# Kernel tuning notes

Measured on AMD Instinct MI355X. Metric: run time of the kernel, lower is better.

## Reference

```python
import jax, jax.numpy as jnp
import numpy as np

B, SEQ_LEN, IN_DIM = 16, 1024, 768
R = 0.1
PI = 3.1415926


def conv1d(x, w, b):
    # x: [B,C,L], w: [O,I,3], 'same' padding, stride 1
    y = jax.lax.conv_general_dilated(x, w, window_strides=(1,), padding=[(1, 1)],
                                     dimension_numbers=('NCH', 'OIH', 'NCH'))
    return y + b[None, :, None]


def layernorm_cl(x, g, b, eps=1e-5):
    # torch nn.LayerNorm((C, L)): normalize jointly over the last two dims of [B,C,L]
    m = x.mean(axis=(1, 2), keepdims=True)
    v = x.var(axis=(1, 2), keepdims=True)
    return (x - m) / jnp.sqrt(v + eps) * g[None] + b[None]


def setup_inputs() -> dict:
    key = jax.random.key(0)
    ks = jax.random.split(key, 8)
    D, D2, L = IN_DIM, IN_DIM * 2, SEQ_LEN
    sc1 = 1.0 / np.sqrt(D * 3)
    sc2 = 1.0 / np.sqrt(D2 * 3)
    return {
        'feats': jax.random.normal(ks[0], (B, L, D), dtype=jnp.float32),
        'conv1_w': jax.random.normal(ks[1], (D2, D, 3), dtype=jnp.float32) * sc1,
        'conv1_b': jnp.zeros((D2,), jnp.float32),
        'ln1_w': jnp.ones((D2, L), jnp.float32),
        'ln1_b': jnp.zeros((D2, L), jnp.float32),
        'conv2_w': jax.random.normal(ks[2], (D2, D2, 3), dtype=jnp.float32) * sc2,
        'conv2_b': jnp.zeros((D2,), jnp.float32),
        'ln2_w': jnp.ones((D2, L), jnp.float32),
        'ln2_b': jnp.zeros((D2, L), jnp.float32),
        'conv3_w': jax.random.normal(ks[3], (2, D2, 3), dtype=jnp.float32) * sc2,
        'conv3_b': jnp.zeros((2,), jnp.float32),
        'ln3_w': jnp.ones((2, L), jnp.float32),
        'ln3_b': jnp.zeros((2, L), jnp.float32),
    }


def reference(feats, conv1_w, conv1_b, ln1_w, ln1_b, conv2_w, conv2_b, ln2_w, ln2_b,
              conv3_w, conv3_b, ln3_w, ln3_b):
    # NOTE: original uses nn.LeakyReLU(True) -> negative_slope=1.0, i.e. identity.
    x = jnp.transpose(feats, (0, 2, 1))                 # [B,D,L]
    h = layernorm_cl(conv1d(x, conv1_w, conv1_b), ln1_w, ln1_b)
    h = layernorm_cl(conv1d(h, conv2_w, conv2_b), ln2_w, ln2_b)
    h = layernorm_cl(conv1d(h, conv3_w, conv3_b), ln3_w, ln3_b)  # [B,2,L]
    s = jax.nn.softmax(h[:, 0, :], axis=1)              # [B,L]
    w = jax.nn.softmax(h[:, 1, :], axis=1)              # [B,L]
    # Vectorized over all centers i: std[b,i] = R*L*s[b,i]
    std = R * SEQ_LEN * s                               # [B,L]
    pos = jnp.arange(SEQ_LEN, dtype=feats.dtype)
    diff2 = (pos[None, :] - pos[:, None]) ** 2          # [i_center, j]
    c = (2.0 * PI) ** -0.5
    gauss = c / std[:, :, None] * jnp.exp(-diff2[None] / (1e-05 + 2.0 * std[:, :, None] ** 2))
    gauss = gauss / jnp.max(gauss, axis=2, keepdims=True)
    att = gauss * w[:, None, :]                         # [B,L_center,L]
    out = jnp.einsum('bij,bjd->bid', att, feats)        # [B,L,D]
    return out
```

## Files before the change

### kernel.cpp

```cpp
#include <hip/hip_runtime.h>
#include <hip/hip_bf16.h>
#include <cstdint>

#define B_   16
#define L_   1024
#define D_   768
#define D2_  1536

typedef __attribute__((ext_vector_type(8))) short bf16x8;
typedef __attribute__((ext_vector_type(4))) float f32x4;

__device__ __forceinline__ float ldin(const void* p, size_t i, int bf) {
  if (bf) return __bfloat162float(((const __hip_bfloat16*)p)[i]);
  return ((const float*)p)[i];
}
__device__ __forceinline__ unsigned short f2bs(float f) {
  __hip_bfloat16 h = __float2bfloat16(f);
  return *(unsigned short*)&h;
}
__device__ __forceinline__ float bs2f(unsigned short u) {
  __hip_bfloat16 h; *(unsigned short*)&h = u;
  return __bfloat162float(h);
}

__device__ __forceinline__ void gload16(const unsigned short* g, unsigned short* l) {
  __builtin_amdgcn_global_load_lds(
      (const __attribute__((address_space(1))) unsigned int*)g,
      (__attribute__((address_space(3))) unsigned int*)l, 16, 0, 0);
}

__global__ void k_detect(const void* __restrict__ ln1w, int* __restrict__ flag) {
  if (threadIdx.x == 0) {
    unsigned u = *(const unsigned*)ln1w;
    *flag = (u == 0x3F800000u) ? 0 : 1;
  }
}

__global__ __launch_bounds__(256) void k_cvt_x(const void* __restrict__ in,
                                               unsigned short* __restrict__ out,
                                               const int* __restrict__ flag) {
  const int bf = *flag;
  const size_t total = (size_t)B_ * (L_ + 2) * D_;
  for (size_t i = (size_t)blockIdx.x * 256 + threadIdx.x; i < total; i += (size_t)gridDim.x * 256) {
    size_t b = i / ((L_ + 2) * D_);
    size_t rem = i - b * ((size_t)(L_ + 2) * D_);
    int pr = (int)(rem / D_);
    int ci = (int)(rem - (size_t)pr * D_);
    float v = 0.f;
    if (pr >= 1 && pr <= L_) v = ldin(in, (b * L_ + pr - 1) * D_ + ci, bf);
    out[i] = f2bs(v);
  }
}

template<int IC>
__global__ __launch_bounds__(256) void k_cvt_w(const void* __restrict__ w,
                                               unsigned short* __restrict__ wp,
                                               const int* __restrict__ flag) {
  const int bf = *flag;
  const int n = D2_ * 3 * IC;
  for (int e = blockIdx.x * 256 + threadIdx.x; e < n; e += gridDim.x * 256) {
    int o = e / (3 * IC); int rem = e - o * 3 * IC;
    int t = rem / IC;     int ci = rem - t * IC;
    wp[e] = f2bs(ldin(w, ((size_t)o * IC + ci) * 3 + t, bf));
  }
}

__global__ __launch_bounds__(256) void k_cvt_lnp(const void* __restrict__ src,
                                                 unsigned short* __restrict__ dst,
                                                 const int* __restrict__ flag) {
  const int bf = *flag;
  __shared__ float t[32][33];
  const int l0 = blockIdx.x * 32, c0 = blockIdx.y * 32;
  const int tx = threadIdx.x, ty = threadIdx.y;
#pragma unroll
  for (int k = 0; k < 4; ++k)
    t[ty + k * 8][tx] = ldin(src, (size_t)(c0 + ty + k * 8) * L_ + l0 + tx, bf);
  __syncthreads();
#pragma unroll
  for (int k = 0; k < 4; ++k)
    dst[(size_t)(l0 + ty + k * 8) * D2_ + c0 + tx] = f2bs(t[tx][ty + k * 8]);
}

__global__ __launch_bounds__(256) void k_zero_hpad(unsigned short* __restrict__ hbp, int G) {
  int i = blockIdx.x * 256 + threadIdx.x;
  int per = 2 * D2_;
  if (i >= G * per) return;
  int lb = i / per; int rem = i - lb * per;
  int w = rem / D2_; int c = rem - w * D2_;
  hbp[((size_t)lb * (L_ + 2) + (size_t)w * (L_ + 1)) * D2_ + c] = 0;
}

template<int IC>
__global__ __launch_bounds__(256, 2) void k_conv_mfma(const unsigned short* __restrict__ x,
                                                      const unsigned short* __restrict__ wp,
                                                      const void* __restrict__ bias,
                                                      unsigned short* __restrict__ hout,
                                                      float* __restrict__ part,
                                                      const int* __restrict__ flag, int b0) {
  __shared__ __attribute__((aligned(16))) unsigned short Xs0[258 * 32];
  __shared__ __attribute__((aligned(16))) unsigned short Xs1[258 * 32];
  __shared__ __attribute__((aligned(16))) unsigned short Ws[3 * 128 * 32];
  __shared__ float rs[4], rss[4];
  const int l0 = blockIdx.x * 256, o0 = blockIdx.y * 128, lb = blockIdx.z;
  const int tid = threadIdx.x;
  const int lane = tid & 63, wid = tid >> 6;
  const int wm = wid >> 1, wn = wid & 1;
  const int lr = lane & 15, lg = lane >> 4;

  f32x4 acc[8][4];
#pragma unroll
  for (int m = 0; m < 8; ++m)
#pragma unroll
    for (int n = 0; n < 4; ++n)
      acc[m][n] = (f32x4){0.f, 0.f, 0.f, 0.f};

  const int sx = ((1 + (tid >> 2)) >> 1) & 3;
  const int sw = (tid >> 3) & 3;
  const unsigned short* xbase = x + ((size_t)lb * (L_ + 2) + l0 + 1 + (tid >> 2)) * IC
                                  + (size_t)((tid & 3) ^ sx) * 8;
  const unsigned short* wbase = wp + (size_t)(o0 + (tid >> 2)) * 3 * IC
                                   + (size_t)((tid & 3) ^ sw) * 8;
  const int hr = (tid >> 2) * 257, hcs = tid & 3;
  const unsigned short* hbase = x + ((size_t)lb * (L_ + 2) + l0 + hr) * IC + hcs * 8;

  auto STAGE_X = [&](unsigned short* Xd, int ci) {
#pragma unroll
    for (int k = 0; k < 4; ++k)
      gload16(xbase + ci + (size_t)k * 64 * IC, Xd + 32 + tid * 8 + k * 2048);
  };
  auto STAGE_W = [&](int ci) {
#pragma unroll
    for (int k = 0; k < 6; ++k)
      gload16(wbase + ci + (size_t)((k & 1) * 192 + (k >> 1)) * IC, Ws + tid * 8 + k * 2048);
  };
  auto COMPUTE = [&](const unsigned short* Xd) {
    const int pb = (((lr >> 1) & 3) ^ lg) * 8;
#pragma unroll
    for (int t = 0; t < 3; ++t) {
      const int pa = ((((lr + t) >> 1) & 3) ^ lg) * 8;
      bf16x8 a[8], b[4];
#pragma unroll
      for (int m = 0; m < 8; ++m)
        a[m] = *(const bf16x8*)&Xd[(wm * 128 + m * 16 + lr + t) * 32 + pa];
#pragma unroll
      for (int n = 0; n < 4; ++n)
        b[n] = *(const bf16x8*)&Ws[(t * 128 + wn * 64 + n * 16 + lr) * 32 + pb];
      __builtin_amdgcn_s_setprio(1);
#pragma unroll
      for (int m = 0; m < 8; ++m)
#pragma unroll
        for (int n = 0; n < 4; ++n)
          acc[m][n] = __builtin_amdgcn_mfma_f32_16x16x32_bf16(a[m], b[n], acc[m][n], 0, 0, 0);
      __builtin_amdgcn_s_setprio(0);
    }
  };

  bf16x8 hreg = {0, 0, 0, 0, 0, 0, 0, 0};
  if (tid < 8) hreg = *(const bf16x8*)(hbase + 0);
  STAGE_X(Xs0, 0);
  STAGE_W(0);
  if (tid < 8) *(bf16x8*)(Xs0 + hr * 32 + hcs * 8) = hreg;
  asm volatile("s_waitcnt vmcnt(0) lgkmcnt(0)" ::: "memory");
  __builtin_amdgcn_s_barrier();

  for (int ci0 = 0; ci0 < IC; ci0 += 64) {
    {
      const int cin = ci0 + 32;
      if (tid < 8) hreg = *(const bf16x8*)(hbase + cin);
      STAGE_X(Xs1, cin);
      COMPUTE(Xs0);
      __builtin_amdgcn_sched_barrier(0);
      __builtin_amdgcn_s_barrier();
      __builtin_amdgcn_sched_barrier(0);
      STAGE_W(cin);
      if (tid < 8) *(bf16x8*)(Xs1 + hr * 32 + hcs * 8) = hreg;
      asm volatile("s_waitcnt vmcnt(0) lgkmcnt(0)" ::: "memory");
      __builtin_amdgcn_s_barrier();
    }
    {
      const int cin = ci0 + 64;
      const bool more = cin < IC;
      if (more) {
        if (tid < 8) hreg = *(const bf16x8*)(hbase + cin);
        STAGE_X(Xs0, cin);
      }
      COMPUTE(Xs1);
      if (more) {
        __builtin_amdgcn_sched_barrier(0);
        __builtin_amdgcn_s_barrier();
        __builtin_amdgcn_sched_barrier(0);
        STAGE_W(cin);
        if (tid < 8) *(bf16x8*)(Xs0 + hr * 32 + hcs * 8) = hreg;
        asm volatile("s_waitcnt vmcnt(0) lgkmcnt(0)" ::: "memory");
        __builtin_amdgcn_s_barrier();
      }
    }
  }

  const int bf = *flag;
  float s = 0.f, ss = 0.f;
  unsigned short* hb = hout + ((size_t)lb * (L_ + 2) + 1) * D2_;
#pragma unroll
  for (int n = 0; n < 4; ++n) {
    int oo = o0 + wn * 64 + n * 16 + lr;
    float bv = ldin(bias, oo, bf);
#pragma unroll
    for (int m = 0; m < 8; ++m) {
      int lbase = l0 + wm * 128 + m * 16 + lg * 4;
#pragma unroll
      for (int j = 0; j < 4; ++j) {
        float v = acc[m][n][j] + bv;
        hb[(size_t)(lbase + j) * D2_ + oo] = f2bs(v);
        s += v; ss += v * v;
      }
    }
  }
#pragma unroll
  for (int o = 32; o > 0; o >>= 1) { s += __shfl_down(s, o); ss += __shfl_down(ss, o); }
  if (lane == 0) { rs[wid] = s; rss[wid] = ss; }
  __syncthreads();
  if (tid == 0) {
    size_t pi = ((size_t)(b0 + lb) * 48 + blockIdx.y * 4 + blockIdx.x) * 2;
    part[pi]     = rs[0] + rs[1] + rs[2] + rs[3];
    part[pi + 1] = rss[0] + rss[1] + rss[2] + rss[3];
  }
}

__global__ void k_stats_final(const float* __restrict__ part, float* __restrict__ stat,
                              int NP, float invN, int b0) {
  const int b = b0 + blockIdx.x;
  float s = 0.f, ss = 0.f;
  for (int p = threadIdx.x; p < NP; p += blockDim.x) {
    s  += part[(size_t)(b * NP + p) * 2];
    ss += part[(size_t)(b * NP + p) * 2 + 1];
  }
#pragma unroll
  for (int o = 32; o > 0; o >>= 1) { s += __shfl_down(s, o); ss += __shfl_down(ss, o); }
  __shared__ float rs[2], rss[2];
  int lane = threadIdx.x & 63, wv = threadIdx.x >> 6;
  if (lane == 0) { rs[wv] = s; rss[wv] = ss; }
  __syncthreads();
  if (threadIdx.x == 0) {
    float m = (rs[0] + rs[1]) * invN;
    float var = (rss[0] + rss[1]) * invN - m * m;
    stat[b * 2] = m;
    stat[b * 2 + 1] = rsqrtf(var + 1e-5f);
  }
}

__global__ __launch_bounds__(256) void k_ln_inplace(unsigned short* __restrict__ hbp,
                                                    const unsigned short* __restrict__ gp,
                                                    const unsigned short* __restrict__ bp,
                                                    const float* __restrict__ stat, int b0) {
  const int lb = blockIdx.y;
  const float m = stat[(b0 + lb) * 2], rstd = stat[(b0 + lb) * 2 + 1];
  const int per8 = D2_ * L_ / 8;
  unsigned short* h = hbp + ((size_t)lb * (L_ + 2) + 1) * D2_;
  for (int e = blockIdx.x * 256 + threadIdx.x; e < per8; e += gridDim.x * 256) {
    bf16x8 v = *(bf16x8*)(h + (size_t)e * 8);
    bf16x8 g = *(const bf16x8*)(gp + (size_t)e * 8);
    bf16x8 bb = *(const bf16x8*)(bp + (size_t)e * 8);
    bf16x8 o;
#pragma unroll
    for (int j = 0; j < 8; ++j)
      o[j] = (short)f2bs((bs2f((unsigned short)v[j]) - m) * rstd * bs2f((unsigned short)g[j])
                         + bs2f((unsigned short)bb[j]));
    *(bf16x8*)(h + (size_t)e * 8) = o;
  }
}

__global__ __launch_bounds__(256) void k_conv3b(const unsigned short* __restrict__ hbp,
                                                const void* __restrict__ w3,
                                                const void* __restrict__ b3,
                                                float* __restrict__ y3,
                                                const int* __restrict__ flag, int b0) {
  __shared__ unsigned short w3s[2 * 3 * D2_];
  const int bf = *flag;
  const int lb = blockIdx.y, gb = b0 + lb;
  const int tid = threadIdx.x, lane = tid & 63, wid = tid >> 6;
  for (int e = tid; e < 2 * 3 * D2_; e += 256) {
    int ch = e / (3 * D2_); int rem = e - ch * 3 * D2_;
    int t = rem / D2_;      int c = rem - t * D2_;
    w3s[e] = f2bs(ldin(w3, ((size_t)ch * D2_ + c) * 3 + t, bf));
  }
  __syncthreads();
  const int l = blockIdx.x * 4 + wid;
  float a0 = 0.f, a1 = 0.f;
#pragma unroll
  for (int t = 0; t < 3; ++t) {
    const unsigned short* hr = hbp + ((size_t)lb * (L_ + 2) + l + t) * D2_;
    const unsigned short* w0 = w3s + t * D2_;
    const unsigned short* w1 = w3s + (3 + t) * D2_;
#pragma unroll
    for (int i = 0; i < 3; ++i) {
      int c0 = (i * 64 + lane) * 8;
      bf16x8 hv  = *(const bf16x8*)(hr + c0);
      bf16x8 wv0 = *(const bf16x8*)(w0 + c0);
      bf16x8 wv1 = *(const bf16x8*)(w1 + c0);
#pragma unroll
      for (int j = 0; j < 8; ++j) {
        float h = bs2f((unsigned short)hv[j]);
        a0 += h * bs2f((unsigned short)wv0[j]);
        a1 += h * bs2f((unsigned short)wv1[j]);
      }
    }
  }
#pragma unroll
  for (int o = 32; o > 0; o >>= 1) { a0 += __shfl_down(a0, o); a1 += __shfl_down(a1, o); }
  if (lane == 0) {
    y3[((size_t)gb * 2) * L_ + l]     = a0 + ldin(b3, 0, bf);
    y3[((size_t)gb * 2 + 1) * L_ + l] = a1 + ldin(b3, 1, bf);
  }
}

__global__ void k_stats3(const float* __restrict__ y3, float* __restrict__ stat3, int b0) {
  const int b = b0 + blockIdx.x;
  const float* p = y3 + (size_t)b * 2 * L_;
  float s = 0.f, ss = 0.f;
  for (int i = threadIdx.x; i < 2 * L_; i += 256) { float v = p[i]; s += v; ss += v * v; }
#pragma unroll
  for (int o = 32; o > 0; o >>= 1) { s += __shfl_down(s, o); ss += __shfl_down(ss, o); }
  __shared__ float rs[4], rss[4];
  int lane = threadIdx.x & 63, wv = threadIdx.x >> 6;
  if (lane == 0) { rs[wv] = s; rss[wv] = ss; }
  __syncthreads();
  if (threadIdx.x == 0) {
    float invN = 1.f / (2 * L_);
    float m = (rs[0] + rs[1] + rs[2] + rs[3]) * invN;
    float var = (rss[0] + rss[1] + rss[2] + rss[3]) * invN - m * m;
    stat3[b * 2] = m;
    stat3[b * 2 + 1] = rsqrtf(var + 1e-5f);
  }
}

__global__ __launch_bounds__(256) void k_softmax(const float* __restrict__ y3,
                                                 const void* __restrict__ g,
                                                 const void* __restrict__ bt,
                                                 const float* __restrict__ stat3,
                                                 float* __restrict__ sw,
                                                 const int* __restrict__ flag, int b0) {
  const int bf = *flag;
  const int ch = blockIdx.x, gb = b0 + blockIdx.y, tid = threadIdx.x;
  const float m = stat3[gb * 2], rstd = stat3[gb * 2 + 1];
  const float* yp = y3 + ((size_t)gb * 2 + ch) * L_;
  float z[4];
  float mx = -1e30f;
#pragma unroll
  for (int k = 0; k < 4; ++k) {
    int l = tid + k * 256;
    z[k] = (yp[l] - m) * rstd * ldin(g, (size_t)ch * L_ + l, bf) + ldin(bt, (size_t)ch * L_ + l, bf);
    mx = fmaxf(mx, z[k]);
  }
#pragma unroll
  for (int o = 32; o > 0; o >>= 1) mx = fmaxf(mx, __shfl_xor(mx, o));
  __shared__ float red[4];
  int lane = tid & 63, wv = tid >> 6;
  if (lane == 0) red[wv] = mx;
  __syncthreads();
  mx = fmaxf(fmaxf(red[0], red[1]), fmaxf(red[2], red[3]));
  float e[4], sum = 0.f;
#pragma unroll
  for (int k = 0; k < 4; ++k) { e[k] = __expf(z[k] - mx); sum += e[k]; }
#pragma unroll
  for (int o = 32; o > 0; o >>= 1) sum += __shfl_xor(sum, o);
  __shared__ float red2[4];
  if (lane == 0) red2[wv] = sum;
  __syncthreads();
  sum = red2[0] + red2[1] + red2[2] + red2[3];
  float inv = 1.f / sum;
#pragma unroll
  for (int k = 0; k < 4; ++k) {
    int l = tid + k * 256;
    sw[((size_t)ch * B_ + gb) * L_ + l] = e[k] * inv;
  }
}

__global__ __launch_bounds__(256) void k_attn(const float* __restrict__ sw,
                                              const void* __restrict__ feats,
                                              void* __restrict__ out,
                                              const int* __restrict__ flag) {
  const int i = blockIdx.x, b = blockIdx.y, tid = threadIdx.x;
  const float s = sw[(size_t)b * L_ + i];
  const float* wv = sw + (size_t)B_ * L_ + (size_t)b * L_;
  const float stdv = 102.4f * s;
  const float denom = 1e-5f + 2.f * stdv * stdv;
  const float inv = 1.f / denom;
  int r = (int)ceilf(sqrtf(30.f * denom));
  int jlo = i - r; if (jlo < 0) jlo = 0;
  int jhi = i + r; if (jhi > L_ - 1) jhi = L_ - 1;
  float a0 = 0.f, a1 = 0.f, a2 = 0.f;
  const int bf = *flag;
  if (bf) {
    const __hip_bfloat16* fb = (const __hip_bfloat16*)feats + (size_t)b * L_ * D_ + tid;
    for (int j = jlo; j <= jhi; ++j) {
      float d = (float)(j - i);
      float gz = __expf(-d * d * inv) * wv[j];
      const __hip_bfloat16* f = fb + (size_t)j * D_;
      a0 += gz * __bfloat162float(f[0]);
      a1 += gz * __bfloat162float(f[256]);
      a2 += gz * __bfloat162float(f[512]);
    }
    __hip_bfloat16* op = (__hip_bfloat16*)out + ((size_t)b * L_ + i) * D_ + tid;
    op[0]   = __float2bfloat16(a0);
    op[256] = __float2bfloat16(a1);
    op[512] = __float2bfloat16(a2);
  } else {
    const float* fb = (const float*)feats + (size_t)b * L_ * D_ + tid;
    for (int j = jlo; j <= jhi; ++j) {
      float d = (float)(j - i);
      float gz = __expf(-d * d * inv) * wv[j];
      const float* f = fb + (size_t)j * D_;
      a0 += gz * f[0];
      a1 += gz * f[256];
      a2 += gz * f[512];
    }
    float* op = (float*)out + ((size_t)b * L_ + i) * D_ + tid;
    op[0] = a0; op[256] = a1; op[512] = a2;
  }
}

extern "C" void kernel_launch(void* const* d_in, const int* in_sizes, int n_in,
                              void* d_out, int out_size, void* d_ws, size_t ws_size,
                              hipStream_t stream) {
  (void)in_sizes; (void)n_in; (void)out_size;
  char* wsb = (char*)d_ws;
  size_t off = 0;
  auto alloc = [&](size_t bytes) -> char* {
    char* p = wsb + off;
    off += (bytes + 255) & ~(size_t)255;
    return p;
  };
  unsigned short* xbp  = (unsigned short*)alloc((size_t)B_ * (L_ + 2) * D_ * 2);
  unsigned short* wp1  = (unsigned short*)alloc((size_t)D2_ * 3 * D_ * 2);
  unsigned short* wp2  = (unsigned short*)alloc((size_t)D2_ * 3 * D2_ * 2);
  unsigned short* lp1w = (unsigned short*)alloc((size_t)D2_ * L_ * 2);
  unsigned short* lp1b = (unsigned short*)alloc((size_t)D2_ * L_ * 2);
  unsigned short* lp2w = (unsigned short*)alloc((size_t)D2_ * L_ * 2);
  unsigned short* lp2b = (unsigned short*)alloc((size_t)D2_ * L_ * 2);
  float* y3   = (float*)alloc((size_t)B_ * 2 * L_ * 4);
  float* swb  = (float*)alloc((size_t)2 * B_ * L_ * 4);
  float* part = (float*)alloc((size_t)B_ * 48 * 2 * 4);
  float* stat = (float*)alloc((size_t)B_ * 2 * 4);
  float* st3  = (float*)alloc((size_t)B_ * 2 * 4);
  int*   flag = (int*)alloc(16);
  const size_t fixed = off;

  int G = 1;
  const int cand[5] = {16, 8, 4, 2, 1};
  for (int k = 0; k < 5; ++k) {
    size_t need = fixed + (size_t)cand[k] * (size_t)(L_ + 2) * D2_ * 2 * 2 + 1024;
    if (need <= ws_size) { G = cand[k]; break; }
  }
  unsigned short* Hbp1 = (unsigned short*)alloc((size_t)G * (L_ + 2) * D2_ * 2);
  unsigned short* Hbp2 = (unsigned short*)alloc((size_t)G * (L_ + 2) * D2_ * 2);

  k_detect<<<1, 64, 0, stream>>>(d_in[3], flag);

  k_cvt_x<<<2048, 256, 0, stream>>>(d_in[0], xbp, flag);
  k_cvt_w<768><<<2048, 256, 0, stream>>>(d_in[1], wp1, flag);
  k_cvt_w<1536><<<2048, 256, 0, stream>>>(d_in[5], wp2, flag);
  dim3 tg(32, 48), tb(32, 8);
  k_cvt_lnp<<<tg, tb, 0, stream>>>(d_in[3], lp1w, flag);
  k_cvt_lnp<<<tg, tb, 0, stream>>>(d_in[4], lp1b, flag);
  k_cvt_lnp<<<tg, tb, 0, stream>>>(d_in[7], lp2w, flag);
  k_cvt_lnp<<<tg, tb, 0, stream>>>(d_in[8], lp2b, flag);
  k_zero_hpad<<<(G * 2 * D2_ + 255) / 256, 256, 0, stream>>>(Hbp1, G);
  k_zero_hpad<<<(G * 2 * D2_ + 255) / 256, 256, 0, stream>>>(Hbp2, G);

  const float invN = 1.f / (float)(D2_ * L_);
  for (int b0 = 0; b0 < B_; b0 += G) {
    k_conv_mfma<768><<<dim3(4, 12, G), 256, 0, stream>>>(
        xbp + (size_t)b0 * (L_ + 2) * D_, wp1, d_in[2], Hbp1, part, flag, b0);
    k_stats_final<<<G, 128, 0, stream>>>(part, stat, 48, invN, b0);
    k_ln_inplace<<<dim3(768, G), 256, 0, stream>>>(Hbp1, lp1w, lp1b, stat, b0);

    k_conv_mfma<1536><<<dim3(4, 12, G), 256, 0, stream>>>(
        Hbp1, wp2, d_in[6], Hbp2, part, flag, b0);
    k_stats_final<<<G, 128, 0, stream>>>(part, stat, 48, invN, b0);
    k_ln_inplace<<<dim3(768, G), 256, 0, stream>>>(Hbp2, lp2w, lp2b, stat, b0);

    k_conv3b<<<dim3(L_ / 4, G), 256, 0, stream>>>(Hbp2, d_in[9], d_in[10], y3, flag, b0);
    k_stats3<<<G, 256, 0, stream>>>(y3, st3, b0);
    k_softmax<<<dim3(2, G), 256, 0, stream>>>(y3, d_in[11], d_in[12], st3, swb, flag, b0);
  }

  k_attn<<<dim3(L_, B_), 256, 0, stream>>>(swb, d_in[0], d_out, flag);
}
```

Before: 505.5 us.

## Widen conv output tile to 192 channels and restructure LN and conv3 grids

The MFMA conv block now computes 192 output channels instead of 128, with six B fragments per warp. A fragments are loaded one at a time inside the m loop to hold register pressure down, and the stats partial count drops to 32. The layernorm kernel now loads gamma and beta once per thread and loops over the batch group rather than reloading them per batch. conv3 processes 16 positions per warp over a smaller grid, amortizing the per-block weight staging into shared memory. The larger accumulator tile (192 floats per lane) risks spills or lower occupancy under launch_bounds(256,2), and the grid becomes coarser.

Result: slower. 1.312 ms (+159.5%).

```diff
diff --git a/kernel.cpp b/kernel.cpp
--- a/kernel.cpp
+++ b/kernel.cpp
@@ -99,19 +99,19 @@
                                                       const int* __restrict__ flag, int b0) {
   __shared__ __attribute__((aligned(16))) unsigned short Xs0[258 * 32];
   __shared__ __attribute__((aligned(16))) unsigned short Xs1[258 * 32];
-  __shared__ __attribute__((aligned(16))) unsigned short Ws[3 * 128 * 32];
+  __shared__ __attribute__((aligned(16))) unsigned short Ws[3 * 192 * 32];
   __shared__ float rs[4], rss[4];
-  const int l0 = blockIdx.x * 256, o0 = blockIdx.y * 128, lb = blockIdx.z;
+  const int l0 = blockIdx.x * 256, o0 = blockIdx.y * 192, lb = blockIdx.z;
   const int tid = threadIdx.x;
   const int lane = tid & 63, wid = tid >> 6;
   const int wm = wid >> 1, wn = wid & 1;
   const int lr = lane & 15, lg = lane >> 4;
 
-  f32x4 acc[8][4];
+  f32x4 acc[8][6];
 #pragma unroll
   for (int m = 0; m < 8; ++m)
 #pragma unroll
-    for (int n = 0; n < 4; ++n)
+    for (int n = 0; n < 6; ++n)
       acc[m][n] = (f32x4){0.f, 0.f, 0.f, 0.f};
 
   const int sx = ((1 + (tid >> 2)) >> 1) & 3;
@@ -130,27 +130,26 @@
   };
   auto STAGE_W = [&](int ci) {
 #pragma unroll
-    for (int k = 0; k < 6; ++k)
-      gload16(wbase + ci + (size_t)((k & 1) * 192 + (k >> 1)) * IC, Ws + tid * 8 + k * 2048);
+    for (int k = 0; k < 9; ++k)
+      gload16(wbase + ci + (size_t)((k % 3) * 64 * 3 + (k / 3)) * IC, Ws + tid * 8 + k * 2048);
   };
   auto COMPUTE = [&](const unsigned short* Xd) {
     const int pb = (((lr >> 1) & 3) ^ lg) * 8;
 #pragma unroll
     for (int t = 0; t < 3; ++t) {
       const int pa = ((((lr + t) >> 1) & 3) ^ lg) * 8;
-      bf16x8 a[8], b[4];
-#pragma unroll
-      for (int m = 0; m < 8; ++m)
-        a[m] = *(const bf16x8*)&Xd[(wm * 128 + m * 16 + lr + t) * 32 + pa];
-#pragma unroll
-      for (int n = 0; n < 4; ++n)
-        b[n] = *(const bf16x8*)&Ws[(t * 128 + wn * 64 + n * 16 + lr) * 32 + pb];
+      bf16x8 b[6];
+#pragma unroll
+      for (int n = 0; n < 6; ++n)
+        b[n] = *(const bf16x8*)&Ws[(t * 192 + wn * 96 + n * 16 + lr) * 32 + pb];
       __builtin_amdgcn_s_setprio(1);
 #pragma unroll
-      for (int m = 0; m < 8; ++m)
-#pragma unroll
-        for (int n = 0; n < 4; ++n)
-          acc[m][n] = __builtin_amdgcn_mfma_f32_16x16x32_bf16(a[m], b[n], acc[m][n], 0, 0, 0);
+      for (int m = 0; m < 8; ++m) {
+        bf16x8 a = *(const bf16x8*)&Xd[(wm * 128 + m * 16 + lr + t) * 32 + pa];
+#pragma unroll
+        for (int n = 0; n < 6; ++n)
+          acc[m][n] = __builtin_amdgcn_mfma_f32_16x16x32_bf16(a, b[n], acc[m][n], 0, 0, 0);
+      }
       __builtin_amdgcn_s_setprio(0);
     }
   };
@@ -201,8 +200,8 @@
   float s = 0.f, ss = 0.f;
   unsigned short* hb = hout + ((size_t)lb * (L_ + 2) + 1) * D2_;
 #pragma unroll
-  for (int n = 0; n < 4; ++n) {
-    int oo = o0 + wn * 64 + n * 16 + lr;
+  for (int n = 0; n < 6; ++n) {
+    int oo = o0 + wn * 96 + n * 16 + lr;
     float bv = ldin(bias, oo, bf);
 #pragma unroll
     for (int m = 0; m < 8; ++m) {
@@ -220,7 +219,7 @@
   if (lane == 0) { rs[wid] = s; rss[wid] = ss; }
   __syncthreads();
   if (tid == 0) {
-    size_t pi = ((size_t)(b0 + lb) * 48 + blockIdx.y * 4 + blockIdx.x) * 2;
+    size_t pi = ((size_t)(b0 + lb) * 32 + blockIdx.y * 4 + blockIdx.x) * 2;
     part[pi]     = rs[0] + rs[1] + rs[2] + rs[3];
     part[pi + 1] = rss[0] + rss[1] + rss[2] + rss[3];
   }
@@ -251,21 +250,26 @@
 __global__ __launch_bounds__(256) void k_ln_inplace(unsigned short* __restrict__ hbp,
                                                     const unsigned short* __restrict__ gp,
                                                     const unsigned short* __restrict__ bp,
-                                                    const float* __restrict__ stat, int b0) {
-  const int lb = blockIdx.y;
-  const float m = stat[(b0 + lb) * 2], rstd = stat[(b0 + lb) * 2 + 1];
-  const int per8 = D2_ * L_ / 8;
-  unsigned short* h = hbp + ((size_t)lb * (L_ + 2) + 1) * D2_;
-  for (int e = blockIdx.x * 256 + threadIdx.x; e < per8; e += gridDim.x * 256) {
-    bf16x8 v = *(bf16x8*)(h + (size_t)e * 8);
-    bf16x8 g = *(const bf16x8*)(gp + (size_t)e * 8);
-    bf16x8 bb = *(const bf16x8*)(bp + (size_t)e * 8);
+                                                    const float* __restrict__ stat,
+                                                    int G, int b0) {
+  const int e = blockIdx.x * 256 + threadIdx.x;
+  bf16x8 g = *(const bf16x8*)(gp + (size_t)e * 8);
+  bf16x8 bb = *(const bf16x8*)(bp + (size_t)e * 8);
+  float gf[8], bf_[8];
+#pragma unroll
+  for (int j = 0; j < 8; ++j) {
+    gf[j] = bs2f((unsigned short)g[j]);
+    bf_[j] = bs2f((unsigned short)bb[j]);
+  }
+  for (int lb = 0; lb < G; ++lb) {
+    const float m = stat[(b0 + lb) * 2], rstd = stat[(b0 + lb) * 2 + 1];
+    unsigned short* h = hbp + ((size_t)lb * (L_ + 2) + 1) * D2_ + (size_t)e * 8;
+    bf16x8 v = *(bf16x8*)h;
     bf16x8 o;
 #pragma unroll
     for (int j = 0; j < 8; ++j)
-      o[j] = (short)f2bs((bs2f((unsigned short)v[j]) - m) * rstd * bs2f((unsigned short)g[j])
-                         + bs2f((unsigned short)bb[j]));
-    *(bf16x8*)(h + (size_t)e * 8) = o;
+      o[j] = (short)f2bs((bs2f((unsigned short)v[j]) - m) * rstd * gf[j] + bf_[j]);
+    *(bf16x8*)h = o;
   }
 }
 
@@ -284,32 +288,36 @@
     w3s[e] = f2bs(ldin(w3, ((size_t)ch * D2_ + c) * 3 + t, bf));
   }
   __syncthreads();
-  const int l = blockIdx.x * 4 + wid;
-  float a0 = 0.f, a1 = 0.f;
-#pragma unroll
-  for (int t = 0; t < 3; ++t) {
-    const unsigned short* hr = hbp + ((size_t)lb * (L_ + 2) + l + t) * D2_;
-    const unsigned short* w0 = w3s + t * D2_;
-    const unsigned short* w1 = w3s + (3 + t) * D2_;
-#pragma unroll
-    for (int i = 0; i < 3; ++i) {
-      int c0 = (i * 64 + lane) * 8;
-      bf16x8 hv  = *(const bf16x8*)(hr + c0);
-      bf16x8 wv0 = *(const bf16x8*)(w0 + c0);
-      bf16x8 wv1 = *(const bf16x8*)(w1 + c0);
-#pragma unroll
-      for (int j = 0; j < 8; ++j) {
-        float h = bs2f((unsigned short)hv[j]);
-        a0 += h * bs2f((unsigned short)wv0[j]);
-        a1 += h * bs2f((unsigned short)wv1[j]);
+  const float bv0 = ldin(b3, 0, bf), bv1 = ldin(b3, 1, bf);
+  const int lbase = blockIdx.x * 64 + wid * 16;
+  for (int li = 0; li < 16; ++li) {
+    const int l = lbase + li;
+    float a0 = 0.f, a1 = 0.f;
+#pragma unroll
+    for (int t = 0; t < 3; ++t) {
+      const unsigned short* hrow = hbp + ((size_t)lb * (L_ + 2) + l + t) * D2_;
+      const unsigned short* w0 = w3s + t * D2_;
+      const unsigned short* w1 = w3s + (3 + t) * D2_;
+#pragma unroll
+      for (int i = 0; i < 3; ++i) {
+        int c0 = (i * 64 + lane) * 8;
+        bf16x8 hv  = *(const bf16x8*)(hrow + c0);
+        bf16x8 wv0 = *(const bf16x8*)(w0 + c0);
+        bf16x8 wv1 = *(const bf16x8*)(w1 + c0);
+#pragma unroll
+        for (int j = 0; j < 8; ++j) {
+          float h = bs2f((unsigned short)hv[j]);
+          a0 += h * bs2f((unsigned short)wv0[j]);
+          a1 += h * bs2f((unsigned short)wv1[j]);
+        }
       }
     }
-  }
-#pragma unroll
-  for (int o = 32; o > 0; o >>= 1) { a0 += __shfl_down(a0, o); a1 += __shfl_down(a1, o); }
-  if (lane == 0) {
-    y3[((size_t)gb * 2) * L_ + l]     = a0 + ldin(b3, 0, bf);
-    y3[((size_t)gb * 2 + 1) * L_ + l] = a1 + ldin(b3, 1, bf);
+#pragma unroll
+    for (int o = 32; o > 0; o >>= 1) { a0 += __shfl_down(a0, o); a1 += __shfl_down(a1, o); }
+    if (lane == 0) {
+      y3[((size_t)gb * 2) * L_ + l]     = a0 + bv0;
+      y3[((size_t)gb * 2 + 1) * L_ + l] = a1 + bv1;
+    }
   }
 }
 
@@ -469,17 +477,17 @@
 
   const float invN = 1.f / (float)(D2_ * L_);
   for (int b0 = 0; b0 < B_; b0 += G) {
-    k_conv_mfma<768><<<dim3(4, 12, G), 256, 0, stream>>>(
+    k_conv_mfma<768><<<dim3(4, 8, G), 256, 0, stream>>>(
         xbp + (size_t)b0 * (L_ + 2) * D_, wp1, d_in[2], Hbp1, part, flag, b0);
-    k_stats_final<<<G, 128, 0, stream>>>(part, stat, 48, invN, b0);
-    k_ln_inplace<<<dim3(768, G), 256, 0, stream>>>(Hbp1, lp1w, lp1b, stat, b0);
-
-    k_conv_mfma<1536><<<dim3(4, 12, G), 256, 0, stream>>>(
+    k_stats_final<<<G, 128, 0, stream>>>(part, stat, 32, invN, b0);
+    k_ln_inplace<<<768, 256, 0, stream>>>(Hbp1, lp1w, lp1b, stat, G, b0);
+
+    k_conv_mfma<1536><<<dim3(4, 8, G), 256, 0, stream>>>(
         Hbp1, wp2, d_in[6], Hbp2, part, flag, b0);
-    k_stats_final<<<G, 128, 0, stream>>>(part, stat, 48, invN, b0);
-    k_ln_inplace<<<dim3(768, G), 256, 0, stream>>>(Hbp2, lp2w, lp2b, stat, b0);
-
-    k_conv3b<<<dim3(L_ / 4, G), 256, 0, stream>>>(Hbp2, d_in[9], d_in[10], y3, flag, b0);
+    k_stats_final<<<G, 128, 0, stream>>>(part, stat, 32, invN, b0);
+    k_ln_inplace<<<768, 256, 0, stream>>>(Hbp2, lp2w, lp2b, stat, G, b0);
+
+    k_conv3b<<<dim3(16, G), 256, 0, stream>>>(Hbp2, d_in[9], d_in[10], y3, flag, b0);
     k_stats3<<<G, 256, 0, stream>>>(y3, st3, b0);
     k_softmax<<<dim3(2, G), 256, 0, stream>>>(y3, d_in[11], d_in[12], st3, swb, flag, b0);
   }
```
